# Kernel tuning notes

Hardware: AMD Instinct MI355X
Metric: run time of the kernel (lower is better)

## Reference

```python
import jax, jax.numpy as jnp
import numpy as np

T, O, K = 256, 64, 16
H, W = 224, 224
D_MODEL, D_OBJ = 768, 2048
GAMMA_INIT = 0.1
OMEGA = 1e-06


def setup_inputs() -> dict:
    key = jax.random.key(0)
    ks = jax.random.split(key, 8)
    obj_feat = jax.random.normal(ks[0], (T, O, D_OBJ), dtype=jnp.float32)
    frame_feat = jax.random.normal(ks[1], (T, D_MODEL), dtype=jnp.float32)
    mark_embeddings = jax.random.normal(ks[2], (K, D_MODEL), dtype=jnp.float32)
    obj_entity = jax.random.randint(ks[3], (T, O), 0, K + 1, dtype=jnp.int32)
    masks = jax.random.randint(ks[4], (T, H, W), 0, K + 1, dtype=jnp.int32)
    # learned params (nn.Linear: y = x @ W.T + b; here stored as [in, out])
    W_obj = jax.random.normal(ks[5], (D_MODEL, D_OBJ), dtype=jnp.float32) / np.sqrt(D_MODEL)
    b_obj = jnp.zeros((D_OBJ,), dtype=jnp.float32)
    W_frame = jax.random.normal(ks[6], (D_MODEL, D_MODEL), dtype=jnp.float32) / np.sqrt(D_MODEL)
    b_frame = jnp.zeros((D_MODEL,), dtype=jnp.float32)
    gamma = jnp.asarray(GAMMA_INIT, dtype=jnp.float32)
    return {
        "obj_feat": obj_feat,
        "frame_feat": frame_feat,
        "mark_embeddings": mark_embeddings,
        "obj_entity": obj_entity,
        "masks": masks,
        "W_obj": W_obj,
        "b_obj": b_obj,
        "W_frame": W_frame,
        "b_frame": b_frame,
        "gamma": gamma,
    }


def reference(obj_feat, frame_feat, mark_embeddings, obj_entity, masks,
              W_obj, b_obj, W_frame, b_frame, gamma):
    # ---- inject_objects: o_hat = o + gamma * P_obj(r_k) (Eq. 4.2) ----
    proj_obj = mark_embeddings @ W_obj + b_obj            # [K, D_OBJ]
    valid = (obj_entity > 0)                              # entity_id == 0 -> no mark
    idx = jnp.clip(obj_entity - 1, 0)                     # [T, O]
    obj_out = obj_feat + gamma * jnp.where(valid[..., None], proj_obj[idx], 0.0)

    # ---- inject_frames: S_t = sum_k (m_k * r_k) / (omega + sum_k m_k) (Eq. 4.3) ----
    Tn, Kn = frame_feat.shape[0], mark_embeddings.shape[0]
    flat = masks.reshape(Tn, -1)                          # [T, H*W]
    seg = (flat + (Kn + 1) * jnp.arange(Tn, dtype=flat.dtype)[:, None]).reshape(-1)
    counts = jax.ops.segment_sum(
        jnp.ones(seg.shape, dtype=jnp.float32), seg, num_segments=Tn * (Kn + 1)
    ).reshape(Tn, Kn + 1)[:, 1:]                          # [T, K] pixel counts per entity
    proj_frame = mark_embeddings @ W_frame + b_frame      # [K, d_model]
    spatial = counts @ proj_frame                         # [T, d_model]
    weight = OMEGA + counts.sum(axis=-1, keepdims=True)   # [T, 1]
    frame_out = frame_feat + gamma * spatial / weight

    return obj_out, frame_out
```

## Files before the change

### kernel.cpp

```cpp
#include <hip/hip_runtime.h>

#define T_N 256
#define O_N 64
#define K_N 16
#define HW_N (224 * 224)
#define DM 768
#define DO 2048
#define OMEGA_F 1e-6f

typedef float f32x4 __attribute__((ext_vector_type(4)));

#define PCOLS 64
#define DSEG 64
#define NSEG (DM / DSEG)
#define NT_O (DO / PCOLS)
#define NT_F (DM / PCOLS)
#define NB_PROJ ((NT_O + NT_F) * NSEG)
#define SUBB 4
#define NB_HIST (T_N * SUBB)
#define NB_OBJ (T_N * O_N / 4)

__global__ __launch_bounds__(256) void proj_kernel(const float* __restrict__ me,
                                                   const float* __restrict__ Wo, const float* __restrict__ bo,
                                                   const float* __restrict__ Wf, const float* __restrict__ bf,
                                                   float* __restrict__ proj_obj, float* __restrict__ proj_frame) {
    __shared__ float partial[4][K_N][PCOLS];
    __shared__ float me_s[K_N * DSEG];
    const int b = blockIdx.x;
    const int tid = threadIdx.x;

    const int tile = b / NSEG, seg = b - tile * NSEG;
    const float* W; const float* bias; float* out; int ld; int j0;
    if (tile < NT_O) { W = Wo; bias = bo; out = proj_obj;   ld = DO; j0 = tile * PCOLS; }
    else             { W = Wf; bias = bf; out = proj_frame; ld = DM; j0 = (tile - NT_O) * PCOLS; }
    const int d0 = seg * DSEG;

    for (int i = tid; i < K_N * DSEG; i += 256) {
        int k = i >> 6, dd = i & 63;
        me_s[i] = me[k * DM + d0 + dd];
    }
    __syncthreads();

    const int jj = tid & (PCOLS - 1);
    const int s  = tid >> 6;
    const int j  = j0 + jj;
    const int db = s * 16;

    float acc[K_N];
    #pragma unroll
    for (int k = 0; k < K_N; ++k) acc[k] = 0.f;

    #pragma unroll
    for (int dd = 0; dd < 16; ++dd) {
        float w = W[(size_t)(d0 + db + dd) * ld + j];
        #pragma unroll
        for (int k = 0; k < K_N; ++k)
            acc[k] += me_s[k * DSEG + db + dd] * w;
    }
    #pragma unroll
    for (int k = 0; k < K_N; ++k) partial[s][k][jj] = acc[k];
    __syncthreads();

    for (int o = tid; o < K_N * PCOLS; o += 256) {
        int k = o >> 6, c = o & 63;
        float v = partial[0][k][c] + partial[1][k][c]
                + partial[2][k][c] + partial[3][k][c];
        if (seg == NSEG - 1) v += bias[j0 + c];
        atomicAdd(&out[k * ld + j0 + c], v);
    }
}

__global__ __launch_bounds__(256) void objhist_kernel(const int* __restrict__ masks,
                                                      float* __restrict__ counts_partial,
                                                      const float* __restrict__ obj_feat,
                                                      const int* __restrict__ obj_entity,
                                                      const float* __restrict__ proj_obj,
                                                      const float* __restrict__ gamma,
                                                      float* __restrict__ obj_out) {
    __shared__ int hist_red[4][16];
    const int b = blockIdx.x;
    const int tid = threadIdx.x;

    if (b < NB_HIST) {
        const int t = b >> 2, sub = b & 3;
        unsigned c0 = 0, c1 = 0, c2 = 0, c3 = 0;
        const int4* p = (const int4*)(masks + (size_t)t * HW_N);
        const int chunk = HW_N / 4 / SUBB;
        const int end = (sub + 1) * chunk;
        for (int i = sub * chunk + tid; i < end; i += 256) {
            int4 v = p[i];
            #define ACC(val) { int u = (val) - 1; \
                unsigned inc = ((val) > 0) ? (1u << ((u & 3) << 3)) : 0u; \
                int q = u >> 2; \
                c0 += (q == 0) ? inc : 0u; c1 += (q == 1) ? inc : 0u; \
                c2 += (q == 2) ? inc : 0u; c3 += (q == 3) ? inc : 0u; }
            ACC(v.x) ACC(v.y) ACC(v.z) ACC(v.w)
            #undef ACC
        }
        unsigned r0 = c0 & 0x00FF00FFu, r1 = (c0 >> 8) & 0x00FF00FFu;
        unsigned r2 = c1 & 0x00FF00FFu, r3 = (c1 >> 8) & 0x00FF00FFu;
        unsigned r4 = c2 & 0x00FF00FFu, r5 = (c2 >> 8) & 0x00FF00FFu;
        unsigned r6 = c3 & 0x00FF00FFu, r7 = (c3 >> 8) & 0x00FF00FFu;
        #pragma unroll
        for (int m = 1; m < 64; m <<= 1) {
            r0 += __shfl_xor(r0, m, 64); r1 += __shfl_xor(r1, m, 64);
            r2 += __shfl_xor(r2, m, 64); r3 += __shfl_xor(r3, m, 64);
            r4 += __shfl_xor(r4, m, 64); r5 += __shfl_xor(r5, m, 64);
            r6 += __shfl_xor(r6, m, 64); r7 += __shfl_xor(r7, m, 64);
        }
        const int wave = tid >> 6, lane = tid & 63;
        if (lane == 0) {
            int* red = hist_red[wave];
            red[0]  = r0 & 0xFFFF; red[1]  = r1 & 0xFFFF; red[2]  = r0 >> 16; red[3]  = r1 >> 16;
            red[4]  = r2 & 0xFFFF; red[5]  = r3 & 0xFFFF; red[6]  = r2 >> 16; red[7]  = r3 >> 16;
            red[8]  = r4 & 0xFFFF; red[9]  = r5 & 0xFFFF; red[10] = r4 >> 16; red[11] = r5 >> 16;
            red[12] = r6 & 0xFFFF; red[13] = r7 & 0xFFFF; red[14] = r6 >> 16; red[15] = r7 >> 16;
        }
        __syncthreads();
        if (tid < K_N) {
            int s = hist_red[0][tid] + hist_red[1][tid]
                  + hist_red[2][tid] + hist_red[3][tid];
            counts_partial[((size_t)sub * T_N + t) * K_N + tid] = (float)s;
        }
    } else {
        const int wave = tid >> 6;
        const int lane = tid & 63;
        const int row = (b - NB_HIST) * 4 + wave;
        const int e = obj_entity[row];
        const float g = gamma[0];
        const f32x4* __restrict__ src = (const f32x4*)(obj_feat + (size_t)row * DO);
        f32x4* __restrict__ dst = (f32x4*)(obj_out + (size_t)row * DO);
        if (e > 0) {
            const f32x4* __restrict__ pr = (const f32x4*)(proj_obj + (size_t)(e - 1) * DO);
            f32x4 a[8], p[8];
            #pragma unroll
            for (int it = 0; it < 8; ++it) a[it] = src[lane + it * 64];
            #pragma unroll
            for (int it = 0; it < 8; ++it) p[it] = pr[lane + it * 64];
            #pragma unroll
            for (int it = 0; it < 8; ++it) {
                f32x4 r = a[it] + g * p[it];
                __builtin_nontemporal_store(r, &dst[lane + it * 64]);
            }
        } else {
            #pragma unroll
            for (int it = 0; it < 8; ++it) {
                f32x4 a = src[lane + it * 64];
                __builtin_nontemporal_store(a, &dst[lane + it * 64]);
            }
        }
    }
}

__global__ __launch_bounds__(256) void frame_kernel(const float* __restrict__ frame_feat,
                                                    const float* __restrict__ counts_partial,
                                                    const float* __restrict__ proj_frame,
                                                    const float* __restrict__ gamma,
                                                    float* __restrict__ frame_out) {
    __shared__ float c[K_N];
    const int t = blockIdx.x;
    const float g = gamma[0];
    if (threadIdx.x < K_N) {
        float s = 0.f;
        #pragma unroll
        for (int sb = 0; sb < SUBB; ++sb)
            s += counts_partial[((size_t)sb * T_N + t) * K_N + threadIdx.x];
        c[threadIdx.x] = s;
    }
    __syncthreads();
    float tot = 0.f;
    #pragma unroll
    for (int k = 0; k < K_N; ++k) tot += c[k];
    const float inv = g / (OMEGA_F + tot);
    for (int j = threadIdx.x; j < DM; j += 256) {
        float acc = 0.f;
        #pragma unroll
        for (int k = 0; k < K_N; ++k) acc += c[k] * proj_frame[k * DM + j];
        frame_out[t * DM + j] = frame_feat[t * DM + j] + acc * inv;
    }
}

extern "C" void kernel_launch(void* const* d_in, const int* in_sizes, int n_in,
                              void* d_out, int out_size, void* d_ws, size_t ws_size,
                              hipStream_t stream) {
    const float* obj_feat   = (const float*)d_in[0];
    const float* frame_feat = (const float*)d_in[1];
    const float* me         = (const float*)d_in[2];
    const int*   obj_entity = (const int*)d_in[3];
    const int*   masks      = (const int*)d_in[4];
    const float* Wo         = (const float*)d_in[5];
    const float* bo         = (const float*)d_in[6];
    const float* Wf         = (const float*)d_in[7];
    const float* bf         = (const float*)d_in[8];
    const float* gamma      = (const float*)d_in[9];

    float* obj_out   = (float*)d_out;
    float* frame_out = (float*)d_out + (size_t)T_N * O_N * DO;

    float* ws = (float*)d_ws;
    float* proj_obj       = ws;
    float* proj_frame     = ws + 32768;
    float* counts_partial = ws + 32768 + 12288;

    hipMemsetAsync(ws, 0, (size_t)(32768 + 12288) * sizeof(float), stream);

    proj_kernel<<<NB_PROJ, 256, 0, stream>>>(me, Wo, bo, Wf, bf, proj_obj, proj_frame);
    objhist_kernel<<<NB_HIST + NB_OBJ, 256, 0, stream>>>(
        masks, counts_partial, obj_feat, obj_entity, proj_obj, gamma, obj_out);
    frame_kernel<<<T_N, 256, 0, stream>>>(frame_feat, counts_partial, proj_frame, gamma, frame_out);
}
```

Measured before the change: 67.82 us.

## Regroup three kernels into two by dependency: projection+histogram, then object+frame outputs

The projection GEMV and the mask histogram are independent, so they now run as one launch, and the object-feature update and the frame update, which both depend on those results, run together in a second launch. This drops one kernel launch and its dependency bubble. In exchange, the bandwidth-heavy histogram no longer overlaps with the object streaming, and the object blocks must now wait for the histogram blocks to finish.

```diff
diff --git a/kernel.cpp b/kernel.cpp
--- a/kernel.cpp
+++ b/kernel.cpp
@@ -20,69 +20,61 @@
 #define NB_HIST (T_N * SUBB)
 #define NB_OBJ (T_N * O_N / 4)
 
-__global__ __launch_bounds__(256) void proj_kernel(const float* __restrict__ me,
-                                                   const float* __restrict__ Wo, const float* __restrict__ bo,
-                                                   const float* __restrict__ Wf, const float* __restrict__ bf,
-                                                   float* __restrict__ proj_obj, float* __restrict__ proj_frame) {
+__global__ __launch_bounds__(256) void fusedA(const float* __restrict__ me,
+                                              const float* __restrict__ Wo, const float* __restrict__ bo,
+                                              const float* __restrict__ Wf, const float* __restrict__ bf,
+                                              const int* __restrict__ masks,
+                                              float* __restrict__ proj_obj, float* __restrict__ proj_frame,
+                                              float* __restrict__ counts_partial) {
     __shared__ float partial[4][K_N][PCOLS];
     __shared__ float me_s[K_N * DSEG];
-    const int b = blockIdx.x;
-    const int tid = threadIdx.x;
-
-    const int tile = b / NSEG, seg = b - tile * NSEG;
-    const float* W; const float* bias; float* out; int ld; int j0;
-    if (tile < NT_O) { W = Wo; bias = bo; out = proj_obj;   ld = DO; j0 = tile * PCOLS; }
-    else             { W = Wf; bias = bf; out = proj_frame; ld = DM; j0 = (tile - NT_O) * PCOLS; }
-    const int d0 = seg * DSEG;
-
-    for (int i = tid; i < K_N * DSEG; i += 256) {
-        int k = i >> 6, dd = i & 63;
-        me_s[i] = me[k * DM + d0 + dd];
-    }
-    __syncthreads();
-
-    const int jj = tid & (PCOLS - 1);
-    const int s  = tid >> 6;
-    const int j  = j0 + jj;
-    const int db = s * 16;
-
-    float acc[K_N];
-    #pragma unroll
-    for (int k = 0; k < K_N; ++k) acc[k] = 0.f;
-
-    #pragma unroll
-    for (int dd = 0; dd < 16; ++dd) {
-        float w = W[(size_t)(d0 + db + dd) * ld + j];
-        #pragma unroll
-        for (int k = 0; k < K_N; ++k)
-            acc[k] += me_s[k * DSEG + db + dd] * w;
-    }
-    #pragma unroll
-    for (int k = 0; k < K_N; ++k) partial[s][k][jj] = acc[k];
-    __syncthreads();
-
-    for (int o = tid; o < K_N * PCOLS; o += 256) {
-        int k = o >> 6, c = o & 63;
-        float v = partial[0][k][c] + partial[1][k][c]
-                + partial[2][k][c] + partial[3][k][c];
-        if (seg == NSEG - 1) v += bias[j0 + c];
-        atomicAdd(&out[k * ld + j0 + c], v);
-    }
-}
-
-__global__ __launch_bounds__(256) void objhist_kernel(const int* __restrict__ masks,
-                                                      float* __restrict__ counts_partial,
-                                                      const float* __restrict__ obj_feat,
-                                                      const int* __restrict__ obj_entity,
-                                                      const float* __restrict__ proj_obj,
-                                                      const float* __restrict__ gamma,
-                                                      float* __restrict__ obj_out) {
     __shared__ int hist_red[4][16];
     const int b = blockIdx.x;
     const int tid = threadIdx.x;
 
-    if (b < NB_HIST) {
-        const int t = b >> 2, sub = b & 3;
+    if (b < NB_PROJ) {
+        const int tile = b / NSEG, seg = b - tile * NSEG;
+        const float* W; const float* bias; float* out; int ld; int j0;
+        if (tile < NT_O) { W = Wo; bias = bo; out = proj_obj;   ld = DO; j0 = tile * PCOLS; }
+        else             { W = Wf; bias = bf; out = proj_frame; ld = DM; j0 = (tile - NT_O) * PCOLS; }
+        const int d0 = seg * DSEG;
+
+        for (int i = tid; i < K_N * DSEG; i += 256) {
+            int k = i >> 6, dd = i & 63;
+            me_s[i] = me[k * DM + d0 + dd];
+        }
+        __syncthreads();
+
+        const int jj = tid & (PCOLS - 1);
+        const int s  = tid >> 6;
+        const int j  = j0 + jj;
+        const int db = s * 16;
+
+        float acc[K_N];
+        #pragma unroll
+        for (int k = 0; k < K_N; ++k) acc[k] = 0.f;
+
+        #pragma unroll
+        for (int dd = 0; dd < 16; ++dd) {
+            float w = W[(size_t)(d0 + db + dd) * ld + j];
+            #pragma unroll
+            for (int k = 0; k < K_N; ++k)
+                acc[k] += me_s[k * DSEG + db + dd] * w;
+        }
+        #pragma unroll
+        for (int k = 0; k < K_N; ++k) partial[s][k][jj] = acc[k];
+        __syncthreads();
+
+        for (int o = tid; o < K_N * PCOLS; o += 256) {
+            int k = o >> 6, c = o & 63;
+            float v = partial[0][k][c] + partial[1][k][c]
+                    + partial[2][k][c] + partial[3][k][c];
+            if (seg == NSEG - 1) v += bias[j0 + c];
+            atomicAdd(&out[k * ld + j0 + c], v);
+        }
+    } else {
+        const int hb = b - NB_PROJ;
+        const int t = hb >> 2, sub = hb & 3;
         unsigned c0 = 0, c1 = 0, c2 = 0, c3 = 0;
         const int4* p = (const int4*)(masks + (size_t)t * HW_N);
         const int chunk = HW_N / 4 / SUBB;
@@ -122,12 +114,28 @@
                   + hist_red[2][tid] + hist_red[3][tid];
             counts_partial[((size_t)sub * T_N + t) * K_N + tid] = (float)s;
         }
-    } else {
+    }
+}
+
+__global__ __launch_bounds__(256) void fusedB(const float* __restrict__ obj_feat,
+                                              const int* __restrict__ obj_entity,
+                                              const float* __restrict__ proj_obj,
+                                              const float* __restrict__ frame_feat,
+                                              const float* __restrict__ counts_partial,
+                                              const float* __restrict__ proj_frame,
+                                              const float* __restrict__ gamma,
+                                              float* __restrict__ obj_out,
+                                              float* __restrict__ frame_out) {
+    __shared__ float c[K_N];
+    const int b = blockIdx.x;
+    const int tid = threadIdx.x;
+    const float g = gamma[0];
+
+    if (b < NB_OBJ) {
         const int wave = tid >> 6;
         const int lane = tid & 63;
-        const int row = (b - NB_HIST) * 4 + wave;
+        const int row = b * 4 + wave;
         const int e = obj_entity[row];
-        const float g = gamma[0];
         const f32x4* __restrict__ src = (const f32x4*)(obj_feat + (size_t)row * DO);
         f32x4* __restrict__ dst = (f32x4*)(obj_out + (size_t)row * DO);
         if (e > 0) {
@@ -149,34 +157,26 @@
                 __builtin_nontemporal_store(a, &dst[lane + it * 64]);
             }
         }
-    }
-}
-
-__global__ __launch_bounds__(256) void frame_kernel(const float* __restrict__ frame_feat,
-                                                    const float* __restrict__ counts_partial,
-                                                    const float* __restrict__ proj_frame,
-                                                    const float* __restrict__ gamma,
-                                                    float* __restrict__ frame_out) {
-    __shared__ float c[K_N];
-    const int t = blockIdx.x;
-    const float g = gamma[0];
-    if (threadIdx.x < K_N) {
-        float s = 0.f;
-        #pragma unroll
-        for (int sb = 0; sb < SUBB; ++sb)
-            s += counts_partial[((size_t)sb * T_N + t) * K_N + threadIdx.x];
-        c[threadIdx.x] = s;
-    }
-    __syncthreads();
-    float tot = 0.f;
-    #pragma unroll
-    for (int k = 0; k < K_N; ++k) tot += c[k];
-    const float inv = g / (OMEGA_F + tot);
-    for (int j = threadIdx.x; j < DM; j += 256) {
-        float acc = 0.f;
-        #pragma unroll
-        for (int k = 0; k < K_N; ++k) acc += c[k] * proj_frame[k * DM + j];
-        frame_out[t * DM + j] = frame_feat[t * DM + j] + acc * inv;
+    } else {
+        const int t = b - NB_OBJ;
+        if (tid < K_N) {
+            float s = 0.f;
+            #pragma unroll
+            for (int sb = 0; sb < SUBB; ++sb)
+                s += counts_partial[((size_t)sb * T_N + t) * K_N + tid];
+            c[tid] = s;
+        }
+        __syncthreads();
+        float tot = 0.f;
+        #pragma unroll
+        for (int k = 0; k < K_N; ++k) tot += c[k];
+        const float inv = g / (OMEGA_F + tot);
+        for (int j = tid; j < DM; j += 256) {
+            float acc = 0.f;
+            #pragma unroll
+            for (int k = 0; k < K_N; ++k) acc += c[k] * proj_frame[k * DM + j];
+            frame_out[t * DM + j] = frame_feat[t * DM + j] + acc * inv;
+        }
     }
 }
 
@@ -204,8 +204,9 @@
 
     hipMemsetAsync(ws, 0, (size_t)(32768 + 12288) * sizeof(float), stream);
 
-    proj_kernel<<<NB_PROJ, 256, 0, stream>>>(me, Wo, bo, Wf, bf, proj_obj, proj_frame);
-    objhist_kernel<<<NB_HIST + NB_OBJ, 256, 0, stream>>>(
-        masks, counts_partial, obj_feat, obj_entity, proj_obj, gamma, obj_out);
-    frame_kernel<<<T_N, 256, 0, stream>>>(frame_feat, counts_partial, proj_frame, gamma, frame_out);
+    fusedA<<<NB_PROJ + NB_HIST, 256, 0, stream>>>(
+        me, Wo, bo, Wf, bf, masks, proj_obj, proj_frame, counts_partial);
+    fusedB<<<NB_OBJ + T_N, 256, 0, stream>>>(
+        obj_feat, obj_entity, proj_obj, frame_feat, counts_partial, proj_frame,
+        gamma, obj_out, frame_out);
 }
```

New measurement: 65.18 us. 3.9% less time.
